# Kernel optimization log

Hardware: AMD Instinct MI355X
Metric: run time of the kernel (lower is better)

## Reference

```python
import jax, jax.numpy as jnp
import numpy as np

NEG_INF = -1e30  # stands in for float('-inf'); avoids nan in masked softmax edge cases


def setup_inputs() -> dict:
    key = jax.random.key(0)
    ks = jax.random.split(key, 6)
    B, N, MD, QD, AD = 64, 512, 1024, 1024, 1024
    stdv_m = 1.0 / np.sqrt(MD)
    stdv_q = 1.0 / np.sqrt(QD)
    stdv_a = 1.0 / np.sqrt(AD)
    return {
        "memory_values": jax.random.normal(ks[0], (B, N, MD), dtype=jnp.float32),
        "mask": jax.random.randint(ks[1], (B, N), 0, 2, dtype=jnp.int32),
        "query": jax.random.normal(ks[2], (B, QD), dtype=jnp.float32),
        "Wh": jax.random.uniform(ks[3], (MD, AD), jnp.float32, -stdv_m, stdv_m),
        "Ws": jax.random.uniform(ks[4], (QD, AD), jnp.float32, -stdv_q, stdv_q),
        "v": jax.random.uniform(ks[5], (AD, 1), jnp.float32, -stdv_a, stdv_a),
    }


def reference(memory_values, mask, query, Wh, Ws, v):
    # Et(i) = tanh(Hi*Wh + St*Ws) @ v ; At = softmax(Et) with masking
    tq = query @ Ws                                   # (B, AD)
    h = jnp.tanh(memory_values @ Wh + tq[:, None, :])  # (B, N, AD)
    logits = jnp.squeeze(h @ v, axis=-1)              # (B, N)

    maskf = mask.astype(logits.dtype)
    # no_cells[b] == 1 iff every cell in row b is masked out
    no_cells = jnp.prod(1.0 - maskf, axis=1, keepdims=True)  # (B, 1)
    suppress = jnp.where(maskf == 0, NEG_INF, 0.0)
    suppress = jnp.where(no_cells == 1.0, 0.0, suppress)
    weights = jax.nn.softmax(logits + suppress, axis=-1)
    weights = jnp.where(no_cells == 1.0, 0.0, weights)

    context = jnp.einsum("bn,bnd->bd", weights, memory_values)
    return context
```

## Files before the change

kernel.cpp:

```cpp
#include <hip/hip_runtime.h>
#include <cstdint>
#include <cstddef>

typedef float floatx4 __attribute__((ext_vector_type(4)));
typedef _Float16 half8_t __attribute__((ext_vector_type(8)));
typedef _Float16 half2_t __attribute__((ext_vector_type(2)));

#define AS1 __attribute__((address_space(1)))
#define AS3 __attribute__((address_space(3)))

__device__ __forceinline__ void glds16(const void* g, void* l) {
  __builtin_amdgcn_global_load_lds((const AS1 void*)g, (AS3 void*)l, 16, 0, 0);
}

__device__ __forceinline__ half2_t pkrtz(float a, float b) {
  return __builtin_bit_cast(half2_t, __builtin_amdgcn_cvt_pkrtz(a, b));
}

__device__ __forceinline__ float fast_tanh(float x) {
  float e2 = __expf(2.f * x);
  return 1.f - 2.f * __builtin_amdgcn_rcpf(e2 + 1.f);
}

__global__ __launch_bounds__(256) void k_prep(
    const float* __restrict__ mem, _Float16* __restrict__ memh,
    const float* __restrict__ Wh, _Float16* __restrict__ WhT,
    const float* __restrict__ q, const float* __restrict__ Ws,
    float* __restrict__ tq) {
  __shared__ float sh[64 * 65];
  const int bx = blockIdx.x;
  const int tid = threadIdx.x;
  if (bx < 16384) {
    size_t i = (((size_t)bx << 8) + tid) << 3;
    floatx4 a = *(const floatx4*)(mem + i);
    floatx4 b = *(const floatx4*)(mem + i + 4);
    union { half2_t h2[4]; half8_t h8; } u;
    u.h2[0] = half2_t{(_Float16)a[0], (_Float16)a[1]};
    u.h2[1] = half2_t{(_Float16)a[2], (_Float16)a[3]};
    u.h2[2] = half2_t{(_Float16)b[0], (_Float16)b[1]};
    u.h2[3] = half2_t{(_Float16)b[2], (_Float16)b[3]};
    *(half8_t*)(memh + i) = u.h8;
  } else if (bx < 16640) {
    int bb = bx - 16384;
    int n0 = (bb & 15) << 6, k0 = (bb >> 4) << 6;
    int tx = tid & 63, ty = tid >> 6;
    #pragma unroll
    for (int r = ty; r < 64; r += 4) sh[r * 65 + tx] = Wh[(size_t)(k0 + r) * 1024 + n0 + tx];
    __syncthreads();
    #pragma unroll
    for (int r = ty; r < 64; r += 4)
      WhT[(size_t)(n0 + r) * 1024 + k0 + tx] = (_Float16)sh[tx * 65 + r];
  } else {
    int bb = bx - 16640;
    int d0 = (bb & 15) << 6, b = bb >> 4;
    int dl = tid & 63, kg = tid >> 6;
    float* qs = sh;
    float* red = sh + 1024;
    for (int k = tid; k < 1024; k += 256) qs[k] = q[(b << 10) + k];
    __syncthreads();
    float acc = 0.f;
    int kbase = kg << 8;
    #pragma unroll 8
    for (int k = 0; k < 256; ++k)
      acc += qs[kbase + k] * Ws[(size_t)(kbase + k) * 1024 + d0 + dl];
    red[(kg << 6) + dl] = acc;
    __syncthreads();
    if (kg == 0)
      tq[(b << 10) + d0 + dl] = red[dl] + red[64 + dl] + red[128 + dl] + red[192 + dl];
  }
}

__global__ void k0_transpose(const float* __restrict__ Wh, _Float16* __restrict__ WhT) {
  __shared__ float t[64][65];
  int k0 = blockIdx.y << 6, n0 = blockIdx.x << 6;
  int tx = threadIdx.x, ty = threadIdx.y;
  #pragma unroll
  for (int r = ty; r < 64; r += 4) t[r][tx] = Wh[(size_t)(k0 + r) * 1024 + n0 + tx];
  __syncthreads();
  #pragma unroll
  for (int r = ty; r < 64; r += 4)
    WhT[(size_t)(n0 + r) * 1024 + k0 + tx] = (_Float16)t[tx][r];
}

__global__ __launch_bounds__(256) void k1_tq(const float* __restrict__ q,
                                             const float* __restrict__ Ws,
                                             float* __restrict__ tq) {
  __shared__ float qs[1024];
  __shared__ float red[4][64];
  int b = blockIdx.y;
  int d0 = blockIdx.x << 6;
  int dl = threadIdx.x & 63, kg = threadIdx.x >> 6;
  for (int k = threadIdx.x; k < 1024; k += 256) qs[k] = q[(b << 10) + k];
  __syncthreads();
  float acc = 0.f;
  int kbase = kg << 8;
  #pragma unroll 8
  for (int k = 0; k < 256; ++k)
    acc += qs[kbase + k] * Ws[(size_t)(kbase + k) * 1024 + d0 + dl];
  red[kg][dl] = acc;
  __syncthreads();
  if (kg == 0)
    tq[(b << 10) + d0 + dl] = red[0][dl] + red[1][dl] + red[2][dl] + red[3][dl];
}

__global__ __launch_bounds__(512, 2) void k2_8ph(
    const _Float16* __restrict__ Ah, const _Float16* __restrict__ BT,
    const float* __restrict__ tq, const float* __restrict__ v,
    float* __restrict__ partials) {
  extern __shared__ char smem[];
  const int bid = blockIdx.x;
  const int wg = ((bid & 7) << 6) | (bid >> 3);
  const int mtile = wg >> 2, ntile = wg & 3;
  const int m0 = mtile << 8, n0 = ntile << 8;
  const int tid = threadIdx.x;
  const int w = tid >> 6, lane = tid & 63;
  const int wm = w >> 2, wn = w & 3, quad = lane >> 4, l15 = lane & 15;

  int aoff[2][4], boff[2][2];
  #pragma unroll
  for (int ks = 0; ks < 2; ++ks) {
    int swz = ((ks << 2) + quad) ^ (l15 & 7);
    #pragma unroll
    for (int i = 0; i < 4; ++i)
      aoff[ks][i] = (wm << 14) + (((i << 4) + l15) << 7) + (swz << 4);
    #pragma unroll
    for (int j = 0; j < 2; ++j)
      boff[ks][j] = 65536 + (wn << 12) + (((j << 4) + l15) << 7) + (swz << 4);
  }

  const int rr = tid >> 3, cc = tid & 7;
  const int r5 = rr & 31;
  int aSrc[2][2], bSrc[2][2], dA[2][2], dB[2][2];
  #pragma unroll
  for (int h = 0; h < 2; ++h)
    #pragma unroll
    for (int hm = 0; hm < 2; ++hm) {
      aSrc[h][hm] = ((m0 + (hm << 7) + (h << 6) + rr) << 10) + ((cc ^ (rr & 7)) << 3);
      dA[h][hm] = (((hm << 1) + h) << 13) + (w << 10);
    }
  #pragma unroll
  for (int ch = 0; ch < 2; ++ch)
    #pragma unroll
    for (int is = 0; is < 2; ++is) {
      int wnb = (is << 1) + (rr >> 5);
      bSrc[ch][is] = ((n0 + (wnb << 6) + (ch << 5) + r5) << 10) + ((cc ^ (r5 & 7)) << 3);
      dB[ch][is] = 65536 + (ch << 14) + (is << 13) + (w << 10);
    }

  floatx4 acc[8][4];
  #pragma unroll
  for (int i = 0; i < 8; ++i)
    #pragma unroll
    for (int j = 0; j < 4; ++j) acc[i][j] = floatx4{0.f, 0.f, 0.f, 0.f};

  half8_t af[2][4], bf[2][2][2];

#define STAGE_A(H, KST, OO)                                   \
  glds16(Ah + aSrc[H][0] + (KST), smem + (OO) + dA[H][0]);    \
  glds16(Ah + aSrc[H][1] + (KST), smem + (OO) + dA[H][1]);
#define STAGE_B(CH, KST, OO)                                  \
  glds16(BT + bSrc[CH][0] + (KST), smem + (OO) + dB[CH][0]);  \
  glds16(BT + bSrc[CH][1] + (KST), smem + (OO) + dB[CH][1]);
#define VMCNT4 asm volatile("s_waitcnt vmcnt(4)" ::: "memory");
#define LOAD_AF(CO, RHOFF)                                    \
  _Pragma("unroll")                                           \
  for (int ks_ = 0; ks_ < 2; ++ks_) {                         \
    _Pragma("unroll")                                         \
    for (int i_ = 0; i_ < 4; ++i_)                            \
      af[ks_][i_] = *(const half8_t*)(smem + (CO) + (RHOFF) + aoff[ks_][i_]); \
  }
#define LOAD_BF(CH, CO, CHOFF)                                \
  _Pragma("unroll")                                           \
  for (int ks_ = 0; ks_ < 2; ++ks_) {                         \
    _Pragma("unroll")                                         \
    for (int j_ = 0; j_ < 2; ++j_)                            \
      bf[CH][ks_][j_] = *(const half8_t*)(smem + (CO) + (CHOFF) + boff[ks_][j_]); \
  }
#define PHASE(RH, CH)                                         \
  __builtin_amdgcn_s_barrier();                               \
  asm volatile("s_waitcnt lgkmcnt(0)" ::: "memory");          \
  __builtin_amdgcn_s_setprio(1);                              \
  _Pragma("unroll")                                           \
  for (int i_ = 0; i_ < 4; ++i_) {                            \
    _Pragma("unroll")                                         \
    for (int j_ = 0; j_ < 2; ++j_)                            \
      acc[(RH)*4 + i_][(CH)*2 + j_] = __builtin_amdgcn_mfma_f32_16x16x32_f16( \
          af[0][i_], bf[CH][0][j_], acc[(RH)*4 + i_][(CH)*2 + j_], 0, 0, 0);  \
  }                                                           \
  _Pragma("unroll")                                           \
  for (int i_ = 0; i_ < 4; ++i_) {                            \
    _Pragma("unroll")                                         \
    for (int j_ = 0; j_ < 2; ++j_)                            \
      acc[(RH)*4 + i_][(CH)*2 + j_] = __builtin_amdgcn_mfma_f32_16x16x32_f16( \
          af[1][i_], bf[CH][1][j_], acc[(RH)*4 + i_][(CH)*2 + j_], 0, 0, 0);  \
  }                                                           \
  __builtin_amdgcn_s_setprio(0);                              \
  __builtin_amdgcn_s_barrier();
#define GROUP(CO, OO, KST)  \
  LOAD_AF(CO, 0)            \
  LOAD_BF(0, CO, 0)         \
  STAGE_A(0, KST, OO)       \
  VMCNT4                    \
  PHASE(0, 0)               \
  LOAD_BF(1, CO, 16384)     \
  STAGE_B(0, KST, OO)       \
  VMCNT4                    \
  PHASE(0, 1)               \
  LOAD_AF(CO, 8192)         \
  STAGE_B(1, KST, OO)       \
  PHASE(1, 0)               \
  STAGE_A(1, KST, OO)       \
  VMCNT4                    \
  PHASE(1, 1)

  STAGE_A(0, 0, 0)
  STAGE_B(0, 0, 0)
  STAGE_B(1, 0, 0)
  STAGE_A(1, 0, 0)
  VMCNT4
  __builtin_amdgcn_s_barrier();

  #pragma unroll 1
  for (int g2 = 0; g2 < 8; ++g2) {
    const int g = g2 << 1;
    const int kst1 = (g + 1) << 6;
    const int kst2 = (g2 == 7) ? (15 << 6) : ((g + 2) << 6);
    GROUP(0, 32768, kst1)
    GROUP(32768, 0, kst2)
  }

#undef GROUP
#undef PHASE
#undef LOAD_BF
#undef LOAD_AF
#undef VMCNT4
#undef STAGE_B
#undef STAGE_A

  asm volatile("s_waitcnt vmcnt(0)" ::: "memory");

  const int b = m0 >> 9;
  const int colb = n0 + (wn << 6) + l15;
  float tqv[4], vv[4];
  #pragma unroll
  for (int jf = 0; jf < 4; ++jf) {
    int n = colb + (jf << 4);
    tqv[jf] = tq[(b << 10) + n];
    vv[jf] = v[n];
  }
  #pragma unroll
  for (int rf = 0; rf < 8; ++rf) {
    #pragma unroll
    for (int r = 0; r < 4; ++r) {
      float s = 0.f;
      #pragma unroll
      for (int jf = 0; jf < 4; ++jf) s += fast_tanh(acc[rf][jf][r] + tqv[jf]) * vv[jf];
      s += __shfl_xor(s, 1);
      s += __shfl_xor(s, 2);
      s += __shfl_xor(s, 4);
      s += __shfl_xor(s, 8);
      if (l15 == 0) {
        int m = m0 + (wm << 7) + (rf << 4) + (quad << 2) + r;
        partials[m * 16 + (ntile << 2) + wn] = s;
      }
    }
  }
}

__global__ __launch_bounds__(256, 2) void k2_gemm_h(
    const _Float16* __restrict__ Ah, const _Float16* __restrict__ BT,
    const float* __restrict__ tq, const float* __restrict__ v,
    float* __restrict__ partials) {
  __shared__ _Float16 As[128 * 32];
  __shared__ _Float16 Bs[128 * 32];
  const int bid = blockIdx.x;
  const int mtile = ((bid >> 6) << 3) | (bid & 7);
  const int nblk = (bid >> 3) & 7;
  const int m0 = mtile << 7, n0 = nblk << 7;
  const int tid = threadIdx.x;
  const int w = tid >> 6, lane = tid & 63;
  const int wm = w >> 1, wn = w & 1, quad = lane >> 4, l15 = lane & 15;

  floatx4 acc[4][4];
  #pragma unroll
  for (int i = 0; i < 4; ++i)
    #pragma unroll
    for (int j = 0; j < 4; ++j) acc[i][j] = floatx4{0.f, 0.f, 0.f, 0.f};

  const _Float16 *gA[2], *gB[2];
  _Float16 *lA[2], *lB[2];
  #pragma unroll
  for (int t = 0; t < 2; ++t) {
    int L = (t << 8) + (w << 6) + lane;
    int row = L >> 2, jj = L & 3;
    int j = (jj - row - (row >> 2)) & 3;
    gA[t] = Ah + (size_t)(m0 + row) * 1024 + (j << 3);
    gB[t] = BT + (size_t)(n0 + row) * 1024 + (j << 3);
    lA[t] = As + (t << 11) + (w << 9);
    lB[t] = Bs + (t << 11) + (w << 9);
  }

  const half8_t *aaddr[4], *baddr[4];
  #pragma unroll
  for (int i = 0; i < 4; ++i) {
    int ar = (wm << 6) + (i << 4) + l15;
    aaddr[i] = (const half8_t*)(As + (ar << 5) + (((quad + ar + (ar >> 2)) & 3) << 3));
    int br = (wn << 6) + (i << 4) + l15;
    baddr[i] = (const half8_t*)(Bs + (br << 5) + (((quad + br + (br >> 2)) & 3) << 3));
  }

  for (int k0 = 0; k0 < 1024; k0 += 32) {
    __syncthreads();
    glds16(gA[0] + k0, lA[0]);
    glds16(gA[1] + k0, lA[1]);
    glds16(gB[0] + k0, lB[0]);
    glds16(gB[1] + k0, lB[1]);
    __syncthreads();
    half8_t af[4], bfr[4];
    #pragma unroll
    for (int i = 0; i < 4; ++i) af[i] = *aaddr[i];
    #pragma unroll
    for (int j = 0; j < 4; ++j) bfr[j] = *baddr[j];
    #pragma unroll
    for (int i = 0; i < 4; ++i)
      #pragma unroll
      for (int j = 0; j < 4; ++j)
        acc[i][j] = __builtin_amdgcn_mfma_f32_16x16x32_f16(af[i], bfr[j], acc[i][j], 0, 0, 0);
  }

  const int b = m0 >> 9;
  const int colbase = n0 + (wn << 6) + l15;
  float tqv[4], vv[4];
  #pragma unroll
  for (int j = 0; j < 4; ++j) {
    int n = colbase + (j << 4);
    tqv[j] = tq[(b << 10) + n];
    vv[j] = v[n];
  }
  #pragma unroll
  for (int i = 0; i < 4; ++i) {
    #pragma unroll
    for (int r = 0; r < 4; ++r) {
      float s = 0.f;
      #pragma unroll
      for (int j = 0; j < 4; ++j) s += fast_tanh(acc[i][j][r] + tqv[j]) * vv[j];
      s += __shfl_xor(s, 1);
      s += __shfl_xor(s, 2);
      s += __shfl_xor(s, 4);
      s += __shfl_xor(s, 8);
      if (l15 == 0) {
        int m = m0 + (wm << 6) + (i << 4) + (quad << 2) + r;
        partials[m * 16 + (nblk << 1) + wn] = s;
      }
    }
  }
}

__global__ __launch_bounds__(256, 2) void k2_gemm_f32(
    const float* __restrict__ A, const _Float16* __restrict__ BT,
    const float* __restrict__ tq, const float* __restrict__ v,
    float* __restrict__ partials) {
  __shared__ float As[128 * 32];
  __shared__ _Float16 Bs[128 * 32];
  const int bid = blockIdx.x;
  const int mtile = ((bid >> 6) << 3) | (bid & 7);
  const int nblk = (bid >> 3) & 7;
  const int m0 = mtile << 7, n0 = nblk << 7;
  const int tid = threadIdx.x;
  const int w = tid >> 6, lane = tid & 63;
  const int wm = w >> 1, wn = w & 1, quad = lane >> 4, l15 = lane & 15;

  floatx4 acc[4][4];
  #pragma unroll
  for (int i = 0; i < 4; ++i)
    #pragma unroll
    for (int j = 0; j < 4; ++j) acc[i][j] = floatx4{0.f, 0.f, 0.f, 0.f};

  const float* gA[4];
  float* lA[4];
  #pragma unroll
  for (int t = 0; t < 4; ++t) {
    int L = (t << 8) + (w << 6) + lane;
    int row = L >> 3, jj = L & 7;
    int j = (jj - row) & 7;
    gA[t] = A + (size_t)(m0 + row) * 1024 + (j << 2);
    lA[t] = As + (t << 10) + (w << 8);
  }
  const _Float16* gB[2];
  _Float16* lB[2];
  #pragma unroll
  for (int t = 0; t < 2; ++t) {
    int L = (t << 8) + (w << 6) + lane;
    int row = L >> 2, jj = L & 3;
    int j = (jj - row - (row >> 2)) & 3;
    gB[t] = BT + (size_t)(n0 + row) * 1024 + (j << 3);
    lB[t] = Bs + (t << 11) + (w << 9);
  }
  const floatx4* aaddr[4][2];
  #pragma unroll
  for (int i = 0; i < 4; ++i) {
    int row = (wm << 6) + (i << 4) + l15;
    #pragma unroll
    for (int h = 0; h < 2; ++h) {
      int pos = ((quad << 1) + h + row) & 7;
      aaddr[i][h] = (const floatx4*)(As + (row << 5) + (pos << 2));
    }
  }
  const half8_t* baddr[4];
  #pragma unroll
  for (int j = 0; j < 4; ++j) {
    int row = (wn << 6) + (j << 4) + l15;
    int pos = (quad + row + (row >> 2)) & 3;
    baddr[j] = (const half8_t*)(Bs + (row << 5) + (pos << 3));
  }
  for (int k0 = 0; k0 < 1024; k0 += 32) {
    __syncthreads();
    glds16(gA[0] + k0, lA[0]);
    glds16(gA[1] + k0, lA[1]);
    glds16(gA[2] + k0, lA[2]);
    glds16(gA[3] + k0, lA[3]);
    glds16(gB[0] + k0, lB[0]);
    glds16(gB[1] + k0, lB[1]);
    __syncthreads();
    half8_t af[4], bfr[4];
    #pragma unroll
    for (int i = 0; i < 4; ++i) {
      floatx4 x = *aaddr[i][0], y = *aaddr[i][1];
      union { half2_t h2[4]; half8_t h8; } u;
      u.h2[0] = pkrtz(x[0], x[1]);
      u.h2[1] = pkrtz(x[2], x[3]);
      u.h2[2] = pkrtz(y[0], y[1]);
      u.h2[3] = pkrtz(y[2], y[3]);
      af[i] = u.h8;
    }
    #pragma unroll
    for (int j = 0; j < 4; ++j) bfr[j] = *baddr[j];
    #pragma unroll
    for (int i = 0; i < 4; ++i)
      #pragma unroll
      for (int j = 0; j < 4; ++j)
        acc[i][j] = __builtin_amdgcn_mfma_f32_16x16x32_f16(af[i], bfr[j], acc[i][j], 0, 0, 0);
  }
  const int b = m0 >> 9;
  const int colbase = n0 + (wn << 6) + l15;
  float tqv[4], vv[4];
  #pragma unroll
  for (int j = 0; j < 4; ++j) {
    int n = colbase + (j << 4);
    tqv[j] = tq[(b << 10) + n];
    vv[j] = v[n];
  }
  #pragma unroll
  for (int i = 0; i < 4; ++i) {
    #pragma unroll
    for (int r = 0; r < 4; ++r) {
      float s = 0.f;
      #pragma unroll
      for (int j = 0; j < 4; ++j) s += fast_tanh(acc[i][j][r] + tqv[j]) * vv[j];
      s += __shfl_xor(s, 1);
      s += __shfl_xor(s, 2);
      s += __shfl_xor(s, 4);
      s += __shfl_xor(s, 8);
      if (l15 == 0) {
        int m = m0 + (wm << 6) + (i << 4) + (quad << 2) + r;
        partials[m * 16 + (nblk << 1) + wn] = s;
      }
    }
  }
}

__global__ __launch_bounds__(512) void k3_softmax(const float* __restrict__ partials,
                                                  const int* __restrict__ mask,
                                                  float* __restrict__ weights) {
  int b = blockIdx.x;
  int n = threadIdx.x;
  int m = (b << 9) + n;
  float s = 0.f;
  #pragma unroll
  for (int i = 0; i < 16; ++i) s += partials[m * 16 + i];
  int mk = mask[m];
  float logit = mk ? s : -1e30f;
  __shared__ float red[8];
  float x = logit;
  #pragma unroll
  for (int off = 32; off > 0; off >>= 1) x = fmaxf(x, __shfl_xor(x, off));
  if ((n & 63) == 0) red[n >> 6] = x;
  __syncthreads();
  float mx = red[0];
  #pragma unroll
  for (int i = 1; i < 8; ++i) mx = fmaxf(mx, red[i]);
  float e = mk ? __expf(logit - mx) : 0.f;
  float ss = e;
  #pragma unroll
  for (int off = 32; off > 0; off >>= 1) ss += __shfl_xor(ss, off);
  __syncthreads();
  if ((n & 63) == 0) red[n >> 6] = ss;
  __syncthreads();
  float tot = 0.f;
  #pragma unroll
  for (int i = 0; i < 8; ++i) tot += red[i];
  weights[m] = (tot > 0.f) ? e / tot : 0.f;
}

__global__ void k4_ctx_h(const _Float16* __restrict__ memh,
                         const float* __restrict__ weights, float* __restrict__ ctxp) {
  int nc = blockIdx.x, b = blockIdx.y;
  int d = threadIdx.x << 3;
  float acc[8] = {0.f, 0.f, 0.f, 0.f, 0.f, 0.f, 0.f, 0.f};
  int nbase = nc << 5;
  for (int n = nbase; n < nbase + 32; ++n) {
    float wv = weights[(b << 9) + n];
    half8_t x = *(const half8_t*)(memh + ((size_t)((b << 9) + n) << 10) + d);
    #pragma unroll
    for (int k = 0; k < 8; ++k) acc[k] += wv * (float)x[k];
  }
  float* o = ctxp + ((size_t)((b << 4) + nc) << 10) + d;
  #pragma unroll
  for (int k = 0; k < 8; ++k) o[k] = acc[k];
}

__global__ void k5_reduce16(const float* __restrict__ ctxp, float* __restrict__ out) {
  int i = (blockIdx.x << 8) + threadIdx.x;
  int b = i >> 10, d = i & 1023;
  float s = 0.f;
  #pragma unroll
  for (int cc = 0; cc < 16; ++cc) s += ctxp[((size_t)((b << 4) + cc) << 10) + d];
  out[i] = s;
}

__global__ void k4_ctx_f32(const float* __restrict__ mem, const float* __restrict__ weights,
                           float* __restrict__ ctxp) {
  int nc = blockIdx.x, b = blockIdx.y;
  int d = threadIdx.x << 3;
  floatx4 a0 = {0.f, 0.f, 0.f, 0.f}, a1 = {0.f, 0.f, 0.f, 0.f};
  int nbase = nc << 6;
  for (int n = nbase; n < nbase + 64; ++n) {
    float wv = weights[(b << 9) + n];
    const floatx4* p = (const floatx4*)(mem + ((size_t)((b << 9) + n) << 10) + d);
    a0 += wv * p[0];
    a1 += wv * p[1];
  }
  floatx4* o = (floatx4*)(ctxp + ((size_t)((b << 3) + nc) << 10) + d);
  o[0] = a0;
  o[1] = a1;
}

__global__ void k5_reduce8(const float* __restrict__ ctxp, float* __restrict__ out) {
  int i = (blockIdx.x << 8) + threadIdx.x;
  int b = i >> 10, d = i & 1023;
  float s = 0.f;
  #pragma unroll
  for (int cc = 0; cc < 8; ++cc) s += ctxp[((size_t)((b << 3) + cc) << 10) + d];
  out[i] = s;
}

extern "C" void kernel_launch(void* const* d_in, const int* in_sizes, int n_in,
                              void* d_out, int out_size, void* d_ws, size_t ws_size,
                              hipStream_t stream) {
  const float* mem = (const float*)d_in[0];
  const int* mask = (const int*)d_in[1];
  const float* query = (const float*)d_in[2];
  const float* Wh = (const float*)d_in[3];
  const float* Ws = (const float*)d_in[4];
  const float* v = (const float*)d_in[5];
  float* out = (float*)d_out;

  char* ws = (char*)d_ws;
  const size_t need16 = (73ull << 20);

  if (ws_size >= need16) {
    _Float16* memh = (_Float16*)ws;
    _Float16* WhT = (_Float16*)(ws + (64ull << 20));
    float* partials = (float*)(ws + (66ull << 20));
    float* tq = (float*)(ws + (68ull << 20));
    float* weights = (float*)(ws + (68ull << 20) + (256 << 10));
    float* ctxp = (float*)(ws + (69ull << 20));

    static int use8 = -1;
    if (use8 < 0) {
      use8 = (hipFuncSetAttribute((const void*)k2_8ph,
                                  hipFuncAttributeMaxDynamicSharedMemorySize,
                                  131072) == hipSuccess) ? 1 : 0;
    }

    k_prep<<<17664, 256, 0, stream>>>(mem, memh, Wh, WhT, query, Ws, tq);
    if (use8)
      k2_8ph<<<512, 512, 131072, stream>>>(memh, WhT, tq, v, partials);
    else
      k2_gemm_h<<<2048, 256, 0, stream>>>(memh, WhT, tq, v, partials);
    k3_softmax<<<64, 512, 0, stream>>>(partials, mask, weights);
    k4_ctx_h<<<dim3(16, 64), 128, 0, stream>>>(memh, weights, ctxp);
    k5_reduce16<<<256, 256, 0, stream>>>(ctxp, out);
  } else {
    _Float16* WhT = (_Float16*)ws;
    float* partials = (float*)(ws + ((size_t)2 << 20));
    float* tq = (float*)(ws + ((size_t)4 << 20));
    float* weights = (float*)(ws + ((size_t)4 << 20) + (256 << 10));
    float* ctxp = (float*)(ws + ((size_t)9 << 19));

    k0_transpose<<<dim3(16, 16), dim3(64, 4), 0, stream>>>(Wh, WhT);
    k1_tq<<<dim3(16, 64), 256, 0, stream>>>(query, Ws, tq);
    k2_gemm_f32<<<2048, 256, 0, stream>>>(mem, WhT, tq, v, partials);
    k3_softmax<<<64, 512, 0, stream>>>(partials, mask, weights);
    k4_ctx_f32<<<dim3(8, 64), 128, 0, stream>>>(mem, weights, ctxp);
    k5_reduce8<<<256, 256, 0, stream>>>(ctxp, out);
  }
}
```

Measured before the change: 306.5 us.

## Restructure GEMM main loop to one barrier per K-step with bulk prefetch

The main GEMM loop now issues all eight global-to-LDS loads for the next K-step up front. It waits until only those eight remain outstanding, then does a single barrier and runs all LDS fragment reads and MFMAs for the current buffer. This replaces the four finely interleaved phases per group, each with its own barriers and lgkmcnt waits. The aim is to cut barrier and synchronisation overhead and give the compiler freedom to overlap LDS reads with MFMAs. The cost is coarser interleaving of global loads with compute, and LDS reads no longer have explicit waits, which relies on compiler-inserted waits.

Measured after the change: 311.3 us. About the same (+1.6%).

```diff
diff --git a/kernel.cpp b/kernel.cpp
--- a/kernel.cpp
+++ b/kernel.cpp
@@ -161,7 +161,7 @@
 #define STAGE_B(CH, KST, OO)                                  \
   glds16(BT + bSrc[CH][0] + (KST), smem + (OO) + dB[CH][0]);  \
   glds16(BT + bSrc[CH][1] + (KST), smem + (OO) + dB[CH][1]);
-#define VMCNT4 asm volatile("s_waitcnt vmcnt(4)" ::: "memory");
+#define VMCNT8 asm volatile("s_waitcnt vmcnt(8)" ::: "memory");
 #define LOAD_AF(CO, RHOFF)                                    \
   _Pragma("unroll")                                           \
   for (int ks_ = 0; ks_ < 2; ++ks_) {                         \
@@ -176,64 +176,57 @@
     for (int j_ = 0; j_ < 2; ++j_)                            \
       bf[CH][ks_][j_] = *(const half8_t*)(smem + (CO) + (CHOFF) + boff[ks_][j_]); \
   }
-#define PHASE(RH, CH)                                         \
+#define MFMAS(RH, CH)                                         \
+  _Pragma("unroll")                                           \
+  for (int ks_ = 0; ks_ < 2; ++ks_) {                         \
+    _Pragma("unroll")                                         \
+    for (int i_ = 0; i_ < 4; ++i_) {                          \
+      _Pragma("unroll")                                       \
+      for (int j_ = 0; j_ < 2; ++j_)                          \
+        acc[(RH)*4 + i_][(CH)*2 + j_] = __builtin_amdgcn_mfma_f32_16x16x32_f16( \
+            af[ks_][i_], bf[CH][ks_][j_], acc[(RH)*4 + i_][(CH)*2 + j_], 0, 0, 0); \
+    }                                                         \
+  }
+#define GROUPN(CO, OO, KST)                                   \
+  STAGE_A(0, KST, OO)                                         \
+  STAGE_B(0, KST, OO)                                         \
+  STAGE_B(1, KST, OO)                                         \
+  STAGE_A(1, KST, OO)                                         \
+  VMCNT8                                                      \
   __builtin_amdgcn_s_barrier();                               \
-  asm volatile("s_waitcnt lgkmcnt(0)" ::: "memory");          \
+  asm volatile("" ::: "memory");                              \
   __builtin_amdgcn_s_setprio(1);                              \
-  _Pragma("unroll")                                           \
-  for (int i_ = 0; i_ < 4; ++i_) {                            \
-    _Pragma("unroll")                                         \
-    for (int j_ = 0; j_ < 2; ++j_)                            \
-      acc[(RH)*4 + i_][(CH)*2 + j_] = __builtin_amdgcn_mfma_f32_16x16x32_f16( \
-          af[0][i_], bf[CH][0][j_], acc[(RH)*4 + i_][(CH)*2 + j_], 0, 0, 0);  \
-  }                                                           \
-  _Pragma("unroll")                                           \
-  for (int i_ = 0; i_ < 4; ++i_) {                            \
-    _Pragma("unroll")                                         \
-    for (int j_ = 0; j_ < 2; ++j_)                            \
-      acc[(RH)*4 + i_][(CH)*2 + j_] = __builtin_amdgcn_mfma_f32_16x16x32_f16( \
-          af[1][i_], bf[CH][1][j_], acc[(RH)*4 + i_][(CH)*2 + j_], 0, 0, 0);  \
-  }                                                           \
+  LOAD_AF(CO, 0)                                              \
+  LOAD_BF(0, CO, 0)                                           \
+  MFMAS(0, 0)                                                 \
+  LOAD_BF(1, CO, 16384)                                       \
+  MFMAS(0, 1)                                                 \
+  LOAD_AF(CO, 8192)                                           \
+  MFMAS(1, 0)                                                 \
+  MFMAS(1, 1)                                                 \
   __builtin_amdgcn_s_setprio(0);                              \
+  asm volatile("" ::: "memory");                              \
   __builtin_amdgcn_s_barrier();
-#define GROUP(CO, OO, KST)  \
-  LOAD_AF(CO, 0)            \
-  LOAD_BF(0, CO, 0)         \
-  STAGE_A(0, KST, OO)       \
-  VMCNT4                    \
-  PHASE(0, 0)               \
-  LOAD_BF(1, CO, 16384)     \
-  STAGE_B(0, KST, OO)       \
-  VMCNT4                    \
-  PHASE(0, 1)               \
-  LOAD_AF(CO, 8192)         \
-  STAGE_B(1, KST, OO)       \
-  PHASE(1, 0)               \
-  STAGE_A(1, KST, OO)       \
-  VMCNT4                    \
-  PHASE(1, 1)
 
   STAGE_A(0, 0, 0)
   STAGE_B(0, 0, 0)
   STAGE_B(1, 0, 0)
   STAGE_A(1, 0, 0)
-  VMCNT4
-  __builtin_amdgcn_s_barrier();
 
   #pragma unroll 1
   for (int g2 = 0; g2 < 8; ++g2) {
     const int g = g2 << 1;
     const int kst1 = (g + 1) << 6;
     const int kst2 = (g2 == 7) ? (15 << 6) : ((g + 2) << 6);
-    GROUP(0, 32768, kst1)
-    GROUP(32768, 0, kst2)
-  }
-
-#undef GROUP
-#undef PHASE
+    GROUPN(0, 32768, kst1)
+    GROUPN(32768, 0, kst2)
+  }
+
+#undef GROUPN
+#undef MFMAS
 #undef LOAD_BF
 #undef LOAD_AF
-#undef VMCNT4
+#undef VMCNT8
 #undef STAGE_B
 #undef STAGE_A
 
```
